# Kernel tuning notes

Measured on AMD Instinct MI355X. Metric: run time of the kernel, lower is better.

Reference implementation:

```python
import jax, jax.numpy as jnp
import numpy as np


def setup_inputs() -> dict:
    key = jax.random.key(0)
    k1, k2, k3, k4 = jax.random.split(key, 4)
    B, C, H, W = 16, 256, 64, 64
    OUT = 256
    x = jax.random.normal(k1, (B, C, H, W), dtype=jnp.float32)
    context = jax.random.normal(k2, (B, C, H, W), dtype=jnp.float32)
    # conv1: 1x1 Conv2d(in=C, out=OUT) -> weight [OUT, C], bias [OUT]
    w1 = jax.random.normal(k3, (OUT, C), dtype=jnp.float32) * (1.0 / np.sqrt(C))
    b1 = jax.random.normal(k4, (OUT,), dtype=jnp.float32) * 0.01
    return {"x": x, "context": context, "w1": w1, "b1": b1}


def reference(x, context, w1, b1):
    # AdaptiveAvgPool2d((1,1)) over context -> per-(b,c) scalar scale [B, C]
    scale = jnp.mean(context, axis=(2, 3))
    # grouped conv with groups=B*C and 1x1 kernels == per-channel elementwise scale
    depth_feat = x * scale[:, :, None, None]  # [B, C, H, W]
    # 1x1 pointwise conv: contract channel dim
    out = jnp.einsum("bchw,oc->bohw", depth_feat, w1) + b1[None, :, None, None]
    return out
```

## Files before the change

### kernel.cpp

```cpp
#include <hip/hip_runtime.h>
#include <hip/hip_bf16.h>


typedef __attribute__((ext_vector_type(8))) short short8;
typedef __attribute__((ext_vector_type(16))) float f32x16;
typedef __attribute__((ext_vector_type(4))) unsigned int u32x4;

static __device__ __forceinline__ unsigned int bfbits(float f) {
    unsigned int u = __float_as_uint(f);
    return u + 0x7FFFu + ((u >> 16) & 1u);
}

static __device__ __forceinline__ unsigned int pkbf(float lo, float hi) {
#if __has_builtin(__builtin_amdgcn_perm)
    return __builtin_amdgcn_perm(bfbits(hi), bfbits(lo), 0x07060302u);
#else
    return (bfbits(lo) >> 16) | (bfbits(hi) & 0xffff0000u);
#endif
}

static __device__ __forceinline__ void gload16(const void* g, void* l) {
    __builtin_amdgcn_global_load_lds(
        (const __attribute__((address_space(1))) unsigned int*)g,
        (__attribute__((address_space(3))) unsigned int*)l, 16, 0, 0);
}

__global__ __launch_bounds__(256) void scale_kernel(const float* __restrict__ ctx,
                                                    float* __restrict__ scale) {
    const int bc = blockIdx.x;
    const float4* p = (const float4*)(ctx + (size_t)bc * 4096);
    const int t = threadIdx.x;
    float s = 0.f;
#pragma unroll
    for (int k = 0; k < 4; k++) {
        float4 v = p[t + k * 256];
        s += v.x + v.y + v.z + v.w;
    }
#pragma unroll
    for (int off = 32; off > 0; off >>= 1) s += __shfl_down(s, off);
    __shared__ float ws[4];
    if ((t & 63) == 0) ws[t >> 6] = s;
    __syncthreads();
    if (t == 0) scale[bc] = (ws[0] + ws[1] + ws[2] + ws[3]) * (1.0f / 4096.0f);
}

__global__ __launch_bounds__(256) void w2f_kernel(const float* __restrict__ w1,
                                                  const float* __restrict__ scale,
                                                  unsigned short* __restrict__ w2f) {
    const int gt = blockIdx.x * 256 + threadIdx.x;
    const int l = gt & 63;
    const int mt = (gt >> 6) & 7;
    const int ks = (gt >> 9) & 15;
    const int b = gt >> 13;
    const int row = mt * 32 + (l & 31);
    const int c0 = ks * 16 + (l >> 5) * 8;

    const float* wr = w1 + row * 256 + c0;
    const float* sc = scale + b * 256 + c0;
    float4 wv0 = *(const float4*)(wr);
    float4 wv1 = *(const float4*)(wr + 4);
    float4 sv0 = *(const float4*)(sc);
    float4 sv1 = *(const float4*)(sc + 4);

    u32x4 pv;
    pv[0] = pkbf(wv0.x * sv0.x, wv0.y * sv0.y);
    pv[1] = pkbf(wv0.z * sv0.z, wv0.w * sv0.w);
    pv[2] = pkbf(wv1.x * sv1.x, wv1.y * sv1.y);
    pv[3] = pkbf(wv1.z * sv1.z, wv1.w * sv1.w);
    *(u32x4*)(w2f + (size_t)gt * 8) = pv;
}

__global__ __launch_bounds__(256, 3) void gemm_kernel(const float* __restrict__ x,
                                                      const unsigned short* __restrict__ w2f,
                                                      const float* __restrict__ b1,
                                                      float* __restrict__ out) {
    __shared__ float bst[2][4096];

    const int bid = blockIdx.x;
    const int b = bid >> 6;
    const int hw0 = (bid & 63) * 64;
    const int tid = threadIdx.x;
    const int w = tid >> 6;
    const int lane = tid & 63;
    const int l31 = lane & 31;
    const int lh = lane >> 5;
    const int o0 = w * 64;

    const unsigned short* Af = w2f + (size_t)b * 65536;
    const float* Xb = x + (size_t)b * (256 * 4096) + hw0;

#pragma unroll
    for (int i = 0; i < 4; i++) {
        const int idx = i * 256 + tid;
        gload16(Xb + (size_t)(idx >> 4) * 4096 + (idx & 15) * 4, &bst[0][idx * 4]);
    }
    __syncthreads();

    f32x16 acc[2][2];
#pragma unroll
    for (int mtl = 0; mtl < 2; mtl++)
#pragma unroll
        for (int ntl = 0; ntl < 2; ntl++) acc[mtl][ntl] = (f32x16)(0.f);

    const int bbase = lh * 512 + l31;

#pragma unroll
    for (int kt = 0; kt < 4; kt++) {
        if (kt < 3) {
#pragma unroll
            for (int i = 0; i < 4; i++) {
                const int idx = i * 256 + tid;
                gload16(Xb + (size_t)((kt + 1) * 64 + (idx >> 4)) * 4096 + (idx & 15) * 4,
                        &bst[(kt + 1) & 1][idx * 4]);
            }
        }
        const float* bb = bst[kt & 1];

        short8 a[4][2];
#pragma unroll
        for (int sub = 0; sub < 4; sub++)
#pragma unroll
            for (int mtl = 0; mtl < 2; mtl++)
                a[sub][mtl] = *(const short8*)(
                    Af + (((size_t)(kt * 4 + sub) * 8 + (w * 2 + mtl)) * 64 + lane) * 8);

#pragma unroll
        for (int sub = 0; sub < 4; sub++) {
#pragma unroll
            for (int ntl = 0; ntl < 2; ntl++) {
                float bf32[8];
#pragma unroll
                for (int e = 0; e < 8; e++)
                    bf32[e] = bb[bbase + ntl * 32 + sub * 1024 + e * 64];
                u32x4 pv;
#pragma unroll
                for (int j = 0; j < 4; j++) pv[j] = pkbf(bf32[2 * j], bf32[2 * j + 1]);
                short8 bfr = __builtin_bit_cast(short8, pv);
#pragma unroll
                for (int mtl = 0; mtl < 2; mtl++)
                    acc[mtl][ntl] = __builtin_amdgcn_mfma_f32_32x32x16_bf16(
                        a[sub][mtl], bfr, acc[mtl][ntl], 0, 0, 0);
            }
        }
        __syncthreads();
    }

    float* outb = out + (size_t)b * 256 * 4096 + hw0;
#pragma unroll
    for (int mtl = 0; mtl < 2; mtl++)
#pragma unroll
        for (int ntl = 0; ntl < 2; ntl++)
#pragma unroll
            for (int r = 0; r < 16; r++) {
                const int row = o0 + mtl * 32 + (r & 3) + 8 * (r >> 2) + 4 * lh;
                outb[(size_t)row * 4096 + ntl * 32 + l31] = acc[mtl][ntl][r] + b1[row];
            }
}

extern "C" void kernel_launch(void* const* d_in, const int* in_sizes, int n_in,
                              void* d_out, int out_size, void* d_ws, size_t ws_size,
                              hipStream_t stream) {
    const float* x = (const float*)d_in[0];
    const float* context = (const float*)d_in[1];
    const float* w1 = (const float*)d_in[2];
    const float* b1 = (const float*)d_in[3];
    float* out = (float*)d_out;

    float* scale = (float*)d_ws;
    unsigned short* w2f = (unsigned short*)((char*)d_ws + 16384);

    scale_kernel<<<4096, 256, 0, stream>>>(context, scale);
    w2f_kernel<<<512, 256, 0, stream>>>(w1, scale, w2f);
    gemm_kernel<<<1024, 256, 0, stream>>>(x, w2f, b1, out);
}
```

Measured before the change: 42.49 us.

## Triple-buffer the X tile loads in the GEMM with explicit vmcnt waits

The GEMM kernel's X staging in LDS moves from two buffers to three, and the K loop is unrolled by hand. Tiles for steps 0 and 1 are issued before any compute, and each step is guarded by an explicit s_waitcnt vmcnt plus s_barrier instead of __syncthreads. The goal is to keep two global-to-LDS loads in flight while MFMA compute runs, hiding HBM latency and cutting the barriers per block. The cost is 48KB of LDS per block, up from 32KB, which may reduce occupancy. The hand-counted vmcnt values also depend on the compiler issuing the loads in the assumed order.

```diff
diff --git a/kernel.cpp b/kernel.cpp
--- a/kernel.cpp
+++ b/kernel.cpp
@@ -74,7 +74,7 @@
                                                       const unsigned short* __restrict__ w2f,
                                                       const float* __restrict__ b1,
                                                       float* __restrict__ out) {
-    __shared__ float bst[2][4096];
+    __shared__ float bst[3][4096];
 
     const int bid = blockIdx.x;
     const int b = bid >> 6;
@@ -89,13 +89,6 @@
     const unsigned short* Af = w2f + (size_t)b * 65536;
     const float* Xb = x + (size_t)b * (256 * 4096) + hw0;
 
-#pragma unroll
-    for (int i = 0; i < 4; i++) {
-        const int idx = i * 256 + tid;
-        gload16(Xb + (size_t)(idx >> 4) * 4096 + (idx & 15) * 4, &bst[0][idx * 4]);
-    }
-    __syncthreads();
-
     f32x16 acc[2][2];
 #pragma unroll
     for (int mtl = 0; mtl < 2; mtl++)
@@ -104,26 +97,24 @@
 
     const int bbase = lh * 512 + l31;
 
+    auto stage = [&](int kt, int buf) {
 #pragma unroll
-    for (int kt = 0; kt < 4; kt++) {
-        if (kt < 3) {
-#pragma unroll
-            for (int i = 0; i < 4; i++) {
-                const int idx = i * 256 + tid;
-                gload16(Xb + (size_t)((kt + 1) * 64 + (idx >> 4)) * 4096 + (idx & 15) * 4,
-                        &bst[(kt + 1) & 1][idx * 4]);
-            }
+        for (int i = 0; i < 4; i++) {
+            const int idx = i * 256 + tid;
+            gload16(Xb + (size_t)(kt * 64 + (idx >> 4)) * 4096 + (idx & 15) * 4,
+                    &bst[buf][idx * 4]);
         }
-        const float* bb = bst[kt & 1];
-
-        short8 a[4][2];
+    };
+    auto afetch = [&](int kt, short8 a[4][2]) {
 #pragma unroll
         for (int sub = 0; sub < 4; sub++)
 #pragma unroll
             for (int mtl = 0; mtl < 2; mtl++)
                 a[sub][mtl] = *(const short8*)(
                     Af + (((size_t)(kt * 4 + sub) * 8 + (w * 2 + mtl)) * 64 + lane) * 8);
-
+    };
+    auto compute = [&](int buf, short8 a[4][2]) {
+        const float* bb = bst[buf];
 #pragma unroll
         for (int sub = 0; sub < 4; sub++) {
 #pragma unroll
@@ -142,8 +133,38 @@
                         a[sub][mtl], bfr, acc[mtl][ntl], 0, 0, 0);
             }
         }
-        __syncthreads();
-    }
+    };
+
+    short8 a[4][2];
+
+    stage(0, 0);
+    stage(1, 1);
+
+    afetch(0, a);
+    asm volatile("s_waitcnt vmcnt(12)" ::: "memory");
+    __builtin_amdgcn_s_barrier();
+    __builtin_amdgcn_sched_barrier(0);
+    stage(2, 2);
+    compute(0, a);
+
+    afetch(1, a);
+    asm volatile("s_waitcnt vmcnt(12)" ::: "memory");
+    __builtin_amdgcn_s_barrier();
+    __builtin_amdgcn_sched_barrier(0);
+    stage(3, 0);
+    compute(1, a);
+
+    afetch(2, a);
+    asm volatile("s_waitcnt vmcnt(12)" ::: "memory");
+    __builtin_amdgcn_s_barrier();
+    __builtin_amdgcn_sched_barrier(0);
+    compute(2, a);
+
+    afetch(3, a);
+    asm volatile("s_waitcnt vmcnt(8)" ::: "memory");
+    __builtin_amdgcn_s_barrier();
+    __builtin_amdgcn_sched_barrier(0);
+    compute(0, a);
 
     float* outb = out + (size_t)b * 256 * 4096 + hw0;
 #pragma unroll
```

Result: slower. 43.37 us (+2.1%).

## Double GEMM N-tile to 128 columns and swizzle block-to-work mapping

Applied to the files above, without the earlier changes.

Each GEMM block now covers 128 spatial columns instead of 64, doubling the LDS staging buffer and the accumulator tiles. This halves the grid and lets each block reuse the fetched scaled-weight fragments across twice as many MFMAs. Block IDs are remapped with an 8-way interleave across batches. The cost is higher LDS and register use, with occupancy lowered to 2 blocks per SIMD set, and fewer blocks to cover 256 CUs.

```diff
diff --git a/kernel.cpp b/kernel.cpp
--- a/kernel.cpp
+++ b/kernel.cpp
@@ -70,15 +70,16 @@
     *(u32x4*)(w2f + (size_t)gt * 8) = pv;
 }
 
-__global__ __launch_bounds__(256, 3) void gemm_kernel(const float* __restrict__ x,
+__global__ __launch_bounds__(256, 2) void gemm_kernel(const float* __restrict__ x,
                                                       const unsigned short* __restrict__ w2f,
                                                       const float* __restrict__ b1,
                                                       float* __restrict__ out) {
-    __shared__ float bst[2][4096];
+    __shared__ float bst[2][8192];
 
     const int bid = blockIdx.x;
-    const int b = bid >> 6;
-    const int hw0 = (bid & 63) * 64;
+    const int work = (bid & 7) * 64 + (bid >> 3);
+    const int b = work >> 5;
+    const int hw0 = (work & 31) * 128;
     const int tid = threadIdx.x;
     const int w = tid >> 6;
     const int lane = tid & 63;
@@ -89,49 +90,40 @@
     const unsigned short* Af = w2f + (size_t)b * 65536;
     const float* Xb = x + (size_t)b * (256 * 4096) + hw0;
 
-#pragma unroll
-    for (int i = 0; i < 4; i++) {
-        const int idx = i * 256 + tid;
-        gload16(Xb + (size_t)(idx >> 4) * 4096 + (idx & 15) * 4, &bst[0][idx * 4]);
-    }
-    __syncthreads();
-
-    f32x16 acc[2][2];
+    f32x16 acc[2][4];
 #pragma unroll
     for (int mtl = 0; mtl < 2; mtl++)
 #pragma unroll
-        for (int ntl = 0; ntl < 2; ntl++) acc[mtl][ntl] = (f32x16)(0.f);
+        for (int ntl = 0; ntl < 4; ntl++) acc[mtl][ntl] = (f32x16)(0.f);
 
-    const int bbase = lh * 512 + l31;
+    const int bbase = lh * 1024 + l31;
 
+    auto stage = [&](int kt, int buf) {
 #pragma unroll
-    for (int kt = 0; kt < 4; kt++) {
-        if (kt < 3) {
-#pragma unroll
-            for (int i = 0; i < 4; i++) {
-                const int idx = i * 256 + tid;
-                gload16(Xb + (size_t)((kt + 1) * 64 + (idx >> 4)) * 4096 + (idx & 15) * 4,
-                        &bst[(kt + 1) & 1][idx * 4]);
-            }
+        for (int i = 0; i < 8; i++) {
+            const int idx = i * 256 + tid;
+            gload16(Xb + (size_t)(kt * 64 + (idx >> 5)) * 4096 + (idx & 31) * 4,
+                    &bst[buf][idx * 4]);
         }
-        const float* bb = bst[kt & 1];
-
-        short8 a[4][2];
+    };
+    auto afetch = [&](int kt, short8 a[4][2]) {
 #pragma unroll
         for (int sub = 0; sub < 4; sub++)
 #pragma unroll
             for (int mtl = 0; mtl < 2; mtl++)
                 a[sub][mtl] = *(const short8*)(
                     Af + (((size_t)(kt * 4 + sub) * 8 + (w * 2 + mtl)) * 64 + lane) * 8);
-
+    };
+    auto compute = [&](int buf, short8 a[4][2]) {
+        const float* bb = bst[buf];
 #pragma unroll
         for (int sub = 0; sub < 4; sub++) {
 #pragma unroll
-            for (int ntl = 0; ntl < 2; ntl++) {
+            for (int ntl = 0; ntl < 4; ntl++) {
                 float bf32[8];
 #pragma unroll
                 for (int e = 0; e < 8; e++)
-                    bf32[e] = bb[bbase + ntl * 32 + sub * 1024 + e * 64];
+                    bf32[e] = bb[bbase + sub * 2048 + e * 128 + ntl * 32];
                 u32x4 pv;
 #pragma unroll
                 for (int j = 0; j < 4; j++) pv[j] = pkbf(bf32[2 * j], bf32[2 * j + 1]);
@@ -142,6 +134,17 @@
                         a[sub][mtl], bfr, acc[mtl][ntl], 0, 0, 0);
             }
         }
+    };
+
+    stage(0, 0);
+    __syncthreads();
+
+    short8 a[4][2];
+#pragma unroll
+    for (int kt = 0; kt < 4; kt++) {
+        afetch(kt, a);
+        if (kt < 3) stage(kt + 1, (kt + 1) & 1);
+        compute(kt & 1, a);
         __syncthreads();
     }
 
@@ -149,7 +152,7 @@
 #pragma unroll
     for (int mtl = 0; mtl < 2; mtl++)
 #pragma unroll
-        for (int ntl = 0; ntl < 2; ntl++)
+        for (int ntl = 0; ntl < 4; ntl++)
 #pragma unroll
             for (int r = 0; r < 16; r++) {
                 const int row = o0 + mtl * 32 + (r & 3) + 8 * (r >> 2) + 4 * lh;
@@ -171,5 +174,5 @@
 
     scale_kernel<<<4096, 256, 0, stream>>>(context, scale);
     w2f_kernel<<<512, 256, 0, stream>>>(w1, scale, w2f);
-    gemm_kernel<<<1024, 256, 0, stream>>>(x, w2f, b1, out);
+    gemm_kernel<<<512, 256, 0, stream>>>(x, w2f, b1, out);
 }
```

Result: no change. 42.55 us (+0.2%).
